# Kernel tuning notes

Measured on AMD Instinct MI355X. Metric: run time of the kernel, lower is better.

The kernel has to match this reference:

```python
import jax, jax.numpy as jnp
import numpy as np

EPS = 1e-6


def _hungarian(cost):
    """Min-cost rectangular assignment (Kuhn-Munkres with potentials).
    Returns (row_ind, col_ind) matching min(n, m) pairs, like scipy's
    linear_sum_assignment. Cost matrices here are tiny (<= 7x7)."""
    cost = np.asarray(cost, dtype=np.float64)
    transposed = False
    if cost.shape[0] > cost.shape[1]:
        cost = cost.T
        transposed = True
    n, m = cost.shape
    INF = 1e18
    u = np.zeros(n + 1)
    v = np.zeros(m + 1)
    p = np.zeros(m + 1, dtype=np.int64)   # p[j] = row matched to col j (1-indexed)
    way = np.zeros(m + 1, dtype=np.int64)
    for i in range(1, n + 1):
        p[0] = i
        j0 = 0
        minv = np.full(m + 1, INF)
        used = np.zeros(m + 1, dtype=bool)
        while True:
            used[j0] = True
            i0 = p[j0]
            delta = INF
            j1 = 0
            for j in range(1, m + 1):
                if not used[j]:
                    cur = cost[i0 - 1, j - 1] - u[i0] - v[j]
                    if cur < minv[j]:
                        minv[j] = cur
                        way[j] = j0
                    if minv[j] < delta:
                        delta = minv[j]
                        j1 = j
            for j in range(m + 1):
                if used[j]:
                    u[p[j]] += delta
                    v[j] -= delta
                else:
                    minv[j] -= delta
            j0 = j1
            if p[j0] == 0:
                break
        while j0:
            j1 = way[j0]
            p[j0] = p[j1]
            j0 = j1
    rows, cols = [], []
    for j in range(1, m + 1):
        if p[j] != 0:
            rows.append(p[j] - 1)
            cols.append(j - 1)
    if transposed:
        rows, cols = cols, rows
    order = np.argsort(rows)
    return [rows[k] for k in order], [cols[k] for k in order]


def setup_inputs() -> dict:
    key = jax.random.key(0)
    kp, kg, kn = jax.random.split(key, 3)
    B, S, H, W = 32, 8, 256, 256
    pred_attn = jax.random.uniform(kp, (B, S, H, W), dtype=jnp.float32)  # soft slot attention
    gt_masks = jnp.round(jax.random.uniform(kg, (B, S, H, W), dtype=jnp.float32))  # binary GT
    num_objects = jax.random.randint(kn, (B,), 0, 8, dtype=jnp.int32)
    return {"pred_attn": pred_attn, "gt_masks": gt_masks, "num_objects": num_objects}


def _match(dice_mat, num_objects, num_gt):
    """Host-side Hungarian matching on the (negated) dice similarity matrix."""
    cost = -np.asarray(dice_mat)  # (B, P, G)
    nobj = np.asarray(num_objects)
    bi, pi, gi = [], [], []
    for b in range(cost.shape[0]):
        n = int(min(int(nobj[b]), num_gt))
        if n == 0:
            continue
        r, c = _hungarian(cost[b, :, :n])
        bi += [b] * len(r)
        pi += list(r)
        gi += list(c)
    return np.array(bi, np.int64), np.array(pi, np.int64), np.array(gi, np.int64)


def _losses(pred_attn, gt_masks, bi, pi, gi):
    B, S, H, W = pred_attn.shape
    # background dice loss (slot 0)
    bg_p = pred_attn[:, 0].reshape(B, -1)
    bg_g = gt_masks[:, 0].reshape(B, -1)
    inter = (bg_p * bg_g).sum(-1)
    union = bg_p.sum(-1) + bg_g.sum(-1)
    bg_loss = (1.0 - (2.0 * inter + EPS) / (union + EPS)).mean()
    # pairwise dice over all (pred_slot, gt_slot) fg pairs in one einsum
    fg_p = pred_attn[:, 1:].reshape(B, S - 1, -1)  # (B, P, HW)
    fg_g = gt_masks[:, 1:].reshape(B, S - 1, -1)   # (B, G, HW)
    inter_m = jnp.einsum('bpn,bgn->bpg', fg_p, fg_g)
    union_m = fg_p.sum(-1)[:, :, None] + fg_g.sum(-1)[:, None, :]
    dice_m = (2.0 * inter_m + EPS) / (union_m + EPS)  # (B, P, G)
    if bi.size:
        fg_loss = (1.0 - dice_m[bi, pi, gi]).mean()
    else:
        fg_loss = jnp.float32(0.0)
    return bg_loss, fg_loss, dice_m


def reference(pred_attn, gt_masks, num_objects):
    BG_WEIGHT, FG_WEIGHT = 1.0, 1.0
    B, S, H, W = pred_attn.shape
    # build dice similarity matrix once (vectorized; replaces the double loop)
    _, _, dice_m = _losses(pred_attn, gt_masks,
                           np.array([], np.int64), np.array([], np.int64), np.array([], np.int64))
    bi, pi, gi = _match(jax.lax.stop_gradient(dice_m), num_objects, S - 1)
    bg_loss, fg_loss, _ = _losses(pred_attn, gt_masks, bi, pi, gi)
    return BG_WEIGHT * bg_loss + FG_WEIGHT * fg_loss
```

## Files before the change

### kernel.cpp

```cpp
#include <hip/hip_runtime.h>

#define EPSF 1e-6f

__device__ __forceinline__ float wave_sum_to_lane63(float x) {
  x += __int_as_float(__builtin_amdgcn_update_dpp(0, __float_as_int(x), 0x111, 0xf, 0xf, true));
  x += __int_as_float(__builtin_amdgcn_update_dpp(0, __float_as_int(x), 0x112, 0xf, 0xf, true));
  x += __int_as_float(__builtin_amdgcn_update_dpp(0, __float_as_int(x), 0x114, 0xf, 0xf, true));
  x += __int_as_float(__builtin_amdgcn_update_dpp(0, __float_as_int(x), 0x118, 0xf, 0xf, true));
  x += __int_as_float(__builtin_amdgcn_update_dpp(0, __float_as_int(x), 0x142, 0xa, 0xf, false));
  x += __int_as_float(__builtin_amdgcn_update_dpp(0, __float_as_int(x), 0x143, 0xc, 0xf, false));
  return x;
}

__global__ __launch_bounds__(256) void msl_accum(const float* __restrict__ pred,
                                                 const float* __restrict__ gt,
                                                 float* __restrict__ part,
                                                 int HW, int HW4) {
  const int b = blockIdx.y;
  const size_t base = (size_t)b * 8 * (size_t)HW;
  const float* P = pred + base;
  const float* G = gt + base;

  float a_bg = 0.0f;
  float af[7][7];
  float sp[8], sg[8];
#pragma unroll
  for (int p = 0; p < 7; ++p)
#pragma unroll
    for (int g = 0; g < 7; ++g) af[p][g] = 0.0f;
#pragma unroll
  for (int s = 0; s < 8; ++s) { sp[s] = 0.0f; sg[s] = 0.0f; }

  const int stride = blockDim.x * gridDim.x;
  for (int i = blockIdx.x * blockDim.x + threadIdx.x; i < HW4; i += stride) {
    float4 pv[8];
#pragma unroll
    for (int s = 0; s < 8; ++s)
      pv[s] = ((const float4*)(P + (size_t)s * HW))[i];
#pragma unroll
    for (int s = 0; s < 8; ++s)
      sp[s] += (pv[s].x + pv[s].y) + (pv[s].z + pv[s].w);

#pragma unroll
    for (int s = 0; s < 8; ++s) {
      float4 gv = ((const float4*)(G + (size_t)s * HW))[i];
      sg[s] += (gv.x + gv.y) + (gv.z + gv.w);
      if (s == 0) {
        a_bg += pv[0].x * gv.x + pv[0].y * gv.y + pv[0].z * gv.z + pv[0].w * gv.w;
      } else {
#pragma unroll
        for (int p = 0; p < 7; ++p)
          af[p][s - 1] += pv[p + 1].x * gv.x + pv[p + 1].y * gv.y +
                          pv[p + 1].z * gv.z + pv[p + 1].w * gv.w;
      }
    }
  }

  float v[66];
  v[0] = a_bg;
#pragma unroll
  for (int p = 0; p < 7; ++p)
#pragma unroll
    for (int g = 0; g < 7; ++g) v[1 + p * 7 + g] = af[p][g];
#pragma unroll
  for (int s = 0; s < 8; ++s) { v[50 + s] = sp[s]; v[58 + s] = sg[s]; }

  __shared__ float red[4][66];
  const int wave = threadIdx.x >> 6;
  const int lane = threadIdx.x & 63;
#pragma unroll
  for (int k = 0; k < 66; ++k) {
    float x = wave_sum_to_lane63(v[k]);
    if (lane == 63) red[wave][k] = x;
  }
  __syncthreads();

  const int row = blockIdx.y * gridDim.x + blockIdx.x;
  if (threadIdx.x < 66) {
    float s = red[0][threadIdx.x] + red[1][threadIdx.x] +
              red[2][threadIdx.x] + red[3][threadIdx.x];
    part[row * 66 + threadIdx.x] = s;
  }
}

__global__ __launch_bounds__(1024) void msl_final(const float* __restrict__ part,
                                                  const int* __restrict__ nobj,
                                                  float* __restrict__ out,
                                                  int B, int RPB) {
  __shared__ float a[32][68];
  __shared__ float dp[32][130];
  __shared__ float dice[32][52];
  __shared__ float r_bg[32];
  __shared__ float r_ds[32];
  __shared__ int   r_n[32];

  const int batch = threadIdx.x >> 5;
  const int lane  = threadIdx.x & 31;
  const bool act  = (batch < B);

  if (act) {
    for (int k = lane; k < 66; k += 32) {
      float s = 0.0f;
#pragma unroll 4
      for (int r = 0; r < RPB; ++r) s += part[(batch * RPB + r) * 66 + k];
      a[batch][k] = s;
    }
  }
  __syncthreads();

  if (act) {
    for (int k = lane; k < 49; k += 32) {
      int p = k / 7, g = k % 7;
      dice[batch][k] = (2.0f * a[batch][1 + k] + EPSF) /
                       (a[batch][51 + p] + a[batch][59 + g] + EPSF);
    }
    if (lane == 0) {
      float u = a[batch][50] + a[batch][58];
      r_bg[batch] = 1.0f - (2.0f * a[batch][0] + EPSF) / (u + EPSF);
      int n = nobj[batch];
      n = n < 0 ? 0 : (n > 7 ? 7 : n);
      r_n[batch] = n;
      r_ds[batch] = 0.0f;
      dp[batch][0] = 0.0f;
    }
  }
  __syncthreads();
  const int n = act ? r_n[batch] : 0;

  for (int c = 1; c <= 7; ++c) {
    if (act && c <= n) {
      for (int mask = lane; mask < 128; mask += 32) {
        if (__popc(mask) == c) {
          float best = -1e30f;
#pragma unroll
          for (int r = 0; r < 7; ++r) {
            if (mask & (1 << r)) {
              float cand = dp[batch][mask ^ (1 << r)] + dice[batch][r * 7 + (c - 1)];
              best = fmaxf(best, cand);
            }
          }
          dp[batch][mask] = best;
        }
      }
    }
    __syncthreads();
  }

  float best = -1e30f;
  if (act && n > 0) {
    for (int mask = lane; mask < 128; mask += 32)
      if (__popc(mask) == n) best = fmaxf(best, dp[batch][mask]);
  }
#pragma unroll
  for (int off = 16; off > 0; off >>= 1)
    best = fmaxf(best, __shfl_down(best, off, 32));
  if (act && lane == 0 && n > 0) r_ds[batch] = best;
  __syncthreads();

  if (threadIdx.x == 0) {
    float bg = 0.0f, ds = 0.0f;
    int cnt = 0;
    for (int b = 0; b < B; ++b) { bg += r_bg[b]; ds += r_ds[b]; cnt += r_n[b]; }
    float fg = cnt > 0 ? ((float)cnt - ds) / (float)cnt : 0.0f;
    out[0] = bg / (float)B + fg;
  }
}

extern "C" void kernel_launch(void* const* d_in, const int* in_sizes, int n_in,
                              void* d_out, int out_size, void* d_ws, size_t ws_size,
                              hipStream_t stream) {
  const float* pred = (const float*)d_in[0];
  const float* gt   = (const float*)d_in[1];
  const int*   nobj = (const int*)d_in[2];
  float* out = (float*)d_out;

  const int B  = in_sizes[2];
  const int HW = in_sizes[0] / (B * 8);
  const int HW4 = HW / 4;

  float* part = (float*)d_ws;

  const int blocksPerBatch = 16;
  msl_accum<<<dim3(blocksPerBatch, B), dim3(256), 0, stream>>>(pred, gt, part, HW, HW4);

  msl_final<<<dim3(1), dim3(32 * B), 0, stream>>>(part, nobj, out, B, blocksPerBatch);
}
```

Before: 168.0 us.

## Stage input streams through LDS with async double-buffered global_load_lds

Replaces direct per-thread float4 global loads with asynchronous global-to-LDS copies (global_load_lds) into a double-buffered shared-memory tile covering all 16 pred/gt streams. Each block now handles a contiguous region per batch, prefetching the next chunk while computing on the current one, with waitcnt and barriers for synchronisation. The aim is to hide memory latency and keep more loads in flight; the cost is 64KB of LDS per block, which limits occupancy, plus two barriers per step. The loop also assumes HW divides evenly by GRIDX*CHUNK.

```diff
diff --git a/kernel.cpp b/kernel.cpp
--- a/kernel.cpp
+++ b/kernel.cpp
@@ -1,4 +1,5 @@
 #include <hip/hip_runtime.h>
+#include <stdint.h>
 
 #define EPSF 1e-6f
 
@@ -12,14 +13,49 @@
   return x;
 }
 
+#define NSTREAM 16
+#define CHUNK   512
+#define GRIDX   16
+
 __global__ __launch_bounds__(256) void msl_accum(const float* __restrict__ pred,
                                                  const float* __restrict__ gt,
-                                                 float* __restrict__ part,
-                                                 int HW, int HW4) {
-  const int b = blockIdx.y;
-  const size_t base = (size_t)b * 8 * (size_t)HW;
-  const float* P = pred + base;
-  const float* G = gt + base;
+                                                 float* __restrict__ part, int HW) {
+  __shared__ float smem[2 * NSTREAM * CHUNK];
+  __shared__ float red[4][66];
+
+  const int b    = blockIdx.y;
+  const int bx   = blockIdx.x;
+  const int tid  = threadIdx.x;
+  const int wave = tid >> 6;
+  const int lane = tid & 63;
+
+  const size_t base   = (size_t)b * 8 * (size_t)HW;
+  const int    region = bx * (HW / GRIDX);
+  const int    steps  = HW / (GRIDX * CHUNK);
+
+  const float* sbase[4];
+#pragma unroll
+  for (int k = 0; k < 4; ++k) {
+    const int S = wave * 4 + k;
+    const float* src = (S < 8) ? (pred + base + (size_t)S * HW)
+                               : (gt   + base + (size_t)(S - 8) * HW);
+    sbase[k] = src + region;
+  }
+
+  auto issue = [&](int step, int bufIdx) {
+#pragma unroll
+    for (int k = 0; k < 4; ++k) {
+      const int S = wave * 4 + k;
+#pragma unroll
+      for (int c = 0; c < 2; ++c) {
+        const float* gp = sbase[k] + step * CHUNK + c * 256 + lane * 4;
+        float* lp = &smem[bufIdx * (NSTREAM * CHUNK) + S * CHUNK + c * 256];
+        __builtin_amdgcn_global_load_lds(
+            (const __attribute__((address_space(1))) void*)gp,
+            (__attribute__((address_space(3))) void*)lp, 16, 0, 0);
+      }
+    }
+  };
 
   float a_bg = 0.0f;
   float af[7][7];
@@ -31,29 +67,41 @@
 #pragma unroll
   for (int s = 0; s < 8; ++s) { sp[s] = 0.0f; sg[s] = 0.0f; }
 
-  const int stride = blockDim.x * gridDim.x;
-  for (int i = blockIdx.x * blockDim.x + threadIdx.x; i < HW4; i += stride) {
-    float4 pv[8];
-#pragma unroll
-    for (int s = 0; s < 8; ++s)
-      pv[s] = ((const float4*)(P + (size_t)s * HW))[i];
-#pragma unroll
-    for (int s = 0; s < 8; ++s)
-      sp[s] += (pv[s].x + pv[s].y) + (pv[s].z + pv[s].w);
+  issue(0, 0);
+  for (int k = 0; k < steps; ++k) {
+    if (k + 1 < steps) {
+      issue(k + 1, (k + 1) & 1);
+      __builtin_amdgcn_s_waitcnt(0x0F78);
+    } else {
+      __builtin_amdgcn_s_waitcnt(0x0F70);
+    }
+    asm volatile("" ::: "memory");
+    __builtin_amdgcn_s_barrier();
+    asm volatile("" ::: "memory");
+
+    const float* buf = &smem[(k & 1) * (NSTREAM * CHUNK)];
+    const int j = tid * 2;
+    float2 pv[8], gv[8];
+#pragma unroll
+    for (int s = 0; s < 8; ++s) pv[s] = *(const float2*)&buf[s * CHUNK + j];
+#pragma unroll
+    for (int s = 0; s < 8; ++s) gv[s] = *(const float2*)&buf[(8 + s) * CHUNK + j];
 
 #pragma unroll
     for (int s = 0; s < 8; ++s) {
-      float4 gv = ((const float4*)(G + (size_t)s * HW))[i];
-      sg[s] += (gv.x + gv.y) + (gv.z + gv.w);
-      if (s == 0) {
-        a_bg += pv[0].x * gv.x + pv[0].y * gv.y + pv[0].z * gv.z + pv[0].w * gv.w;
-      } else {
-#pragma unroll
-        for (int p = 0; p < 7; ++p)
-          af[p][s - 1] += pv[p + 1].x * gv.x + pv[p + 1].y * gv.y +
-                          pv[p + 1].z * gv.z + pv[p + 1].w * gv.w;
-      }
-    }
+      sp[s] += pv[s].x + pv[s].y;
+      sg[s] += gv[s].x + gv[s].y;
+    }
+    a_bg += pv[0].x * gv[0].x + pv[0].y * gv[0].y;
+#pragma unroll
+    for (int p = 0; p < 7; ++p)
+#pragma unroll
+      for (int g = 0; g < 7; ++g)
+        af[p][g] += pv[p + 1].x * gv[g + 1].x + pv[p + 1].y * gv[g + 1].y;
+
+    asm volatile("" ::: "memory");
+    __builtin_amdgcn_s_barrier();
+    asm volatile("" ::: "memory");
   }
 
   float v[66];
@@ -65,21 +113,17 @@
 #pragma unroll
   for (int s = 0; s < 8; ++s) { v[50 + s] = sp[s]; v[58 + s] = sg[s]; }
 
-  __shared__ float red[4][66];
-  const int wave = threadIdx.x >> 6;
-  const int lane = threadIdx.x & 63;
-#pragma unroll
-  for (int k = 0; k < 66; ++k) {
-    float x = wave_sum_to_lane63(v[k]);
-    if (lane == 63) red[wave][k] = x;
+#pragma unroll
+  for (int kk = 0; kk < 66; ++kk) {
+    float x = wave_sum_to_lane63(v[kk]);
+    if (lane == 63) red[wave][kk] = x;
   }
   __syncthreads();
 
   const int row = blockIdx.y * gridDim.x + blockIdx.x;
-  if (threadIdx.x < 66) {
-    float s = red[0][threadIdx.x] + red[1][threadIdx.x] +
-              red[2][threadIdx.x] + red[3][threadIdx.x];
-    part[row * 66 + threadIdx.x] = s;
+  if (tid < 66) {
+    float s = red[0][tid] + red[1][tid] + red[2][tid] + red[3][tid];
+    part[row * 66 + tid] = s;
   }
 }
 
@@ -176,12 +220,10 @@
 
   const int B  = in_sizes[2];
   const int HW = in_sizes[0] / (B * 8);
-  const int HW4 = HW / 4;
 
   float* part = (float*)d_ws;
 
-  const int blocksPerBatch = 16;
-  msl_accum<<<dim3(blocksPerBatch, B), dim3(256), 0, stream>>>(pred, gt, part, HW, HW4);
-
-  msl_final<<<dim3(1), dim3(32 * B), 0, stream>>>(part, nobj, out, B, blocksPerBatch);
-}
+  msl_accum<<<dim3(GRIDX, B), dim3(256), 0, stream>>>(pred, gt, part, HW);
+
+  msl_final<<<dim3(1), dim3(32 * B), 0, stream>>>(part, nobj, out, B, GRIDX);
+}
```

Measured after the change: 168.8 us. Within noise of the previous version (+0.5%).

## Stage pred tiles into LDS via async global_load_lds and widen grid

Applied to the files above, without the earlier changes.

Each block now owns a fixed 2048-pixel tile per batch and stages all 8 pred slots for that tile into shared memory with direct global-to-LDS loads. The block then streams the GT slots one at a time, prefetching the next slot into registers. The grid grows from 16 to HW/2048 blocks per batch, giving more parallelism and bytes in flight, at the cost of 64KB of LDS per block, which limits occupancy. The kernel assumes HW is a multiple of 2048, and the final reduction now sums more partial rows.

```diff
diff --git a/kernel.cpp b/kernel.cpp
--- a/kernel.cpp
+++ b/kernel.cpp
@@ -1,4 +1,5 @@
 #include <hip/hip_runtime.h>
+#include <stdint.h>
 
 #define EPSF 1e-6f
 
@@ -12,14 +13,44 @@
   return x;
 }
 
+__device__ __forceinline__ float dot4(float4 a, float4 b) {
+  return a.x * b.x + a.y * b.y + a.z * b.z + a.w * b.w;
+}
+__device__ __forceinline__ float sum4(float4 a) {
+  return (a.x + a.y) + (a.z + a.w);
+}
+
+#define RSZ 2048
+
 __global__ __launch_bounds__(256) void msl_accum(const float* __restrict__ pred,
                                                  const float* __restrict__ gt,
-                                                 float* __restrict__ part,
-                                                 int HW, int HW4) {
-  const int b = blockIdx.y;
+                                                 float* __restrict__ part, int HW) {
+  __shared__ float sm[8 * RSZ];
+  const int b    = blockIdx.y;
+  const int bx   = blockIdx.x;
+  const int tid  = threadIdx.x;
+  const int wave = tid >> 6;
+  const int lane = tid & 63;
+
   const size_t base = (size_t)b * 8 * (size_t)HW;
-  const float* P = pred + base;
-  const float* G = gt + base;
+  const float* Pr = pred + base + (size_t)bx * RSZ;
+  const float* Gr = gt   + base + (size_t)bx * RSZ;
+
+#pragma unroll
+  for (int s = 0; s < 8; ++s) {
+    const float* sbase = Pr + (size_t)s * HW;
+#pragma unroll
+    for (int k = 0; k < 2; ++k) {
+      const int chunk = wave * 2 + k;
+      const float* gp = sbase + chunk * 256 + lane * 4;
+      float* lp = &sm[s * RSZ + chunk * 256];
+      __builtin_amdgcn_global_load_lds(
+          (const __attribute__((address_space(1))) void*)gp,
+          (__attribute__((address_space(3))) void*)lp, 16, 0, 0);
+    }
+  }
+  __builtin_amdgcn_s_waitcnt(0x0F70);
+  __syncthreads();
 
   float a_bg = 0.0f;
   float af[7][7];
@@ -31,29 +62,45 @@
 #pragma unroll
   for (int s = 0; s < 8; ++s) { sp[s] = 0.0f; sg[s] = 0.0f; }
 
-  const int stride = blockDim.x * gridDim.x;
-  for (int i = blockIdx.x * blockDim.x + threadIdx.x; i < HW4; i += stride) {
-    float4 pv[8];
-#pragma unroll
-    for (int s = 0; s < 8; ++s)
-      pv[s] = ((const float4*)(P + (size_t)s * HW))[i];
-#pragma unroll
-    for (int s = 0; s < 8; ++s)
-      sp[s] += (pv[s].x + pv[s].y) + (pv[s].z + pv[s].w);
-
-#pragma unroll
-    for (int s = 0; s < 8; ++s) {
-      float4 gv = ((const float4*)(G + (size_t)s * HW))[i];
-      sg[s] += (gv.x + gv.y) + (gv.z + gv.w);
-      if (s == 0) {
-        a_bg += pv[0].x * gv.x + pv[0].y * gv.y + pv[0].z * gv.z + pv[0].w * gv.w;
-      } else {
-#pragma unroll
-        for (int p = 0; p < 7; ++p)
-          af[p][s - 1] += pv[p + 1].x * gv.x + pv[p + 1].y * gv.y +
-                          pv[p + 1].z * gv.z + pv[p + 1].w * gv.w;
-      }
-    }
+  const int t4 = tid * 4;
+
+  {
+    float4 ga = *(const float4*)(Gr + t4);
+    float4 gb = *(const float4*)(Gr + 1024 + t4);
+    sg[0] = sum4(ga) + sum4(gb);
+#pragma unroll
+    for (int p = 0; p < 8; ++p) {
+      float4 pa = *(const float4*)&sm[p * RSZ + t4];
+      float4 pb = *(const float4*)&sm[p * RSZ + 1024 + t4];
+      sp[p] = sum4(pa) + sum4(pb);
+      if (p == 0) a_bg = dot4(pa, ga) + dot4(pb, gb);
+    }
+  }
+
+  float4 ga = *(const float4*)(Gr + (size_t)1 * HW + t4);
+  float4 gb = *(const float4*)(Gr + (size_t)1 * HW + 1024 + t4);
+#pragma unroll 1
+  for (int g = 1; g < 8; ++g) {
+    float4 na, nb;
+    if (g < 7) {
+      na = *(const float4*)(Gr + (size_t)(g + 1) * HW + t4);
+      nb = *(const float4*)(Gr + (size_t)(g + 1) * HW + 1024 + t4);
+    }
+    sg[g] = sum4(ga) + sum4(gb);
+#pragma unroll
+    for (int p = 1; p < 8; ++p) {
+      float4 pa = *(const float4*)&sm[p * RSZ + t4];
+      float4 pb = *(const float4*)&sm[p * RSZ + 1024 + t4];
+      af[p - 1][g - 1] = fmaf(pa.x, ga.x, af[p - 1][g - 1]);
+      af[p - 1][g - 1] = fmaf(pa.y, ga.y, af[p - 1][g - 1]);
+      af[p - 1][g - 1] = fmaf(pa.z, ga.z, af[p - 1][g - 1]);
+      af[p - 1][g - 1] = fmaf(pa.w, ga.w, af[p - 1][g - 1]);
+      af[p - 1][g - 1] = fmaf(pb.x, gb.x, af[p - 1][g - 1]);
+      af[p - 1][g - 1] = fmaf(pb.y, gb.y, af[p - 1][g - 1]);
+      af[p - 1][g - 1] = fmaf(pb.z, gb.z, af[p - 1][g - 1]);
+      af[p - 1][g - 1] = fmaf(pb.w, gb.w, af[p - 1][g - 1]);
+    }
+    ga = na; gb = nb;
   }
 
   float v[66];
@@ -65,21 +112,20 @@
 #pragma unroll
   for (int s = 0; s < 8; ++s) { v[50 + s] = sp[s]; v[58 + s] = sg[s]; }
 
-  __shared__ float red[4][66];
-  const int wave = threadIdx.x >> 6;
-  const int lane = threadIdx.x & 63;
+  __syncthreads();
+  float* red = sm;
 #pragma unroll
   for (int k = 0; k < 66; ++k) {
     float x = wave_sum_to_lane63(v[k]);
-    if (lane == 63) red[wave][k] = x;
+    if (lane == 63) red[wave * 66 + k] = x;
   }
   __syncthreads();
 
   const int row = blockIdx.y * gridDim.x + blockIdx.x;
-  if (threadIdx.x < 66) {
-    float s = red[0][threadIdx.x] + red[1][threadIdx.x] +
-              red[2][threadIdx.x] + red[3][threadIdx.x];
-    part[row * 66 + threadIdx.x] = s;
+  if (tid < 66) {
+    float s = red[0 * 66 + tid] + red[1 * 66 + tid] +
+              red[2 * 66 + tid] + red[3 * 66 + tid];
+    part[row * 66 + tid] = s;
   }
 }
 
@@ -176,12 +222,11 @@
 
   const int B  = in_sizes[2];
   const int HW = in_sizes[0] / (B * 8);
-  const int HW4 = HW / 4;
 
   float* part = (float*)d_ws;
 
-  const int blocksPerBatch = 16;
-  msl_accum<<<dim3(blocksPerBatch, B), dim3(256), 0, stream>>>(pred, gt, part, HW, HW4);
-
-  msl_final<<<dim3(1), dim3(32 * B), 0, stream>>>(part, nobj, out, B, blocksPerBatch);
-}
+  const int GRIDX = HW / RSZ;
+  msl_accum<<<dim3(GRIDX, B), dim3(256), 0, stream>>>(pred, gt, part, HW);
+
+  msl_final<<<dim3(1), dim3(32 * B), 0, stream>>>(part, nobj, out, B, GRIDX);
+}
```

Result: slower. 190.1 us (+13.1%).
